# Performance work log

Measured on AMD Instinct MI355X. Metric: run time of the kernel, lower is better.

The kernel has to match this reference:

```python
import jax, jax.numpy as jnp
import numpy as np
import math

N, T, NS, NO, HID = 256, 1000, 10, 10, 64


def gru_seq(x, Wi, Wh, bi, bh):
    # x: [N,T,D] -> hidden states [N,T,HID] (single-layer GRU, h0 = 0)
    xproj = x @ Wi + bi  # [N,T,3H], precompute input projections
    def step(h, xp):
        hp = h @ Wh + bh
        xr, xz, xn = jnp.split(xp, 3, axis=-1)
        hr, hz, hn = jnp.split(hp, 3, axis=-1)
        r = jax.nn.sigmoid(xr + hr)
        z = jax.nn.sigmoid(xz + hz)
        n = jnp.tanh(xn + r * hn)
        h_new = (1.0 - z) * n + z * h
        return h_new, h_new
    h0 = jnp.zeros((x.shape[0], Wh.shape[0]), x.dtype)
    _, hs = jax.lax.scan(step, h0, jnp.swapaxes(xproj, 0, 1))
    return jnp.swapaxes(hs, 0, 1)


def setup_inputs() -> dict:
    key = jax.random.key(0)
    ks = jax.random.split(key, 12)
    D = NO + NS  # GRU input = concat(y, x_hat)
    s = lambda fan: 1.0 / np.sqrt(fan)
    inp = {
        "Yi_batch": jax.random.normal(ks[0], (N, T, NO), jnp.float32),
        "X_hat_batch": jax.random.normal(ks[1], (N, T, NS), jnp.float32),
        # per-sample observation noise covariance: 0.5*I plus small random diagonal
        "Cw_batch": 0.5 * jnp.eye(NO, dtype=jnp.float32)[None] + jnp.eye(NO)[None] * 0.1 * jax.random.uniform(ks[2], (N, 1, 1), jnp.float32),
        "H": jax.random.normal(ks[3], (NO, NS), jnp.float32) * s(NS),
        "mu_w": jnp.zeros((NO, 1), jnp.float32),
        "Wi": jax.random.normal(ks[4], (D, 3 * HID), jnp.float32) * s(D),
        "Wh": jax.random.normal(ks[5], (HID, 3 * HID), jnp.float32) * s(HID),
        "bi": jnp.zeros((3 * HID,), jnp.float32),
        "bh": jnp.zeros((3 * HID,), jnp.float32),
        "W_mu": jax.random.normal(ks[6], (HID, NS), jnp.float32) * s(HID),
        "b_mu": jnp.zeros((NS,), jnp.float32),
        "W_var": jax.random.normal(ks[7], (HID, NS), jnp.float32) * s(HID),
        "b_var": jnp.zeros((NS,), jnp.float32),
    }
    return inp


def reference(Yi_batch, X_hat_batch, Cw_batch, H, mu_w, Wi, Wh, bi, bh, W_mu, b_mu, W_var, b_var):
    n_obs = Yi_batch.shape[-1]
    Tlen = Yi_batch.shape[1]
    # RNN: mu and (positive) vars per time step
    hs = gru_seq(jnp.concatenate([Yi_batch, X_hat_batch], axis=-1), Wi, Wh, bi, bh)
    mu_prev = hs @ W_mu + b_mu                       # [N,T,NS]
    var_prev = jax.nn.softplus(hs @ W_var + b_var)   # [N,T,NS] diag of L_xt_yt_prev
    # marginal over y: mu_y = H mu_prev + mu_w ; L_y = H diag(var) H^T + Cw
    mu_y = jnp.einsum('ij,ntj->nti', H, mu_prev) + mu_w[:, 0]
    HLH = jnp.einsum('ij,ntj,kj->ntik', H, var_prev, H)   # [N,T,NO,NO]
    L_y = HLH + Cw_batch[:, None]                          # broadcast Cw over time
    e = Yi_batch - mu_y
    # Gaussian log-likelihood via Cholesky (L_y is SPD)
    chol = jnp.linalg.cholesky(L_y)
    logdet = 2.0 * jnp.sum(jnp.log(jnp.diagonal(chol, axis1=-2, axis2=-1)), axis=-1)  # [N,T]
    sol = jnp.linalg.solve(L_y, e[..., None])[..., 0]
    quad = jnp.sum(e * sol, axis=-1)                       # [N,T]
    logprob = (-0.5 * n_obs * Tlen * math.log(2.0 * math.pi)
               - 0.5 * jnp.sum(logdet, axis=1)
               - 0.5 * jnp.sum(quad, axis=1))              # [N]
    return jnp.mean(logprob / (Tlen * n_obs))
```

## Files before the change

kernel.cpp:

```cpp
#include <hip/hip_runtime.h>
#include <math.h>

#define BN 256
#define TT 1000
#define NO 10
#define NS 10
#define HID 64
#define DIN 20
#define G3 192
#define GS 8
#define NG 125
#define SPW 16
#define NBLK (BN / SPW)

using bf16x8 = __attribute__((ext_vector_type(8))) short;
using f32x4  = __attribute__((ext_vector_type(4))) float;

__device__ __forceinline__ float rcpf(float x) { return __builtin_amdgcn_rcpf(x); }
__device__ __forceinline__ void sync_lds() {
    asm volatile("s_waitcnt lgkmcnt(0)\n\ts_barrier" ::: "memory");
}
__device__ __forceinline__ unsigned cvt_pk_bf16(float a, float b) {
    unsigned r;
    asm("v_cvt_pk_bf16_f32 %0, %1, %2" : "=v"(r) : "v"(a), "v"(b));
    return r;
}
__device__ __forceinline__ short f2bf(float f) {
    unsigned u = __float_as_uint(f);
    return (short)((u + 0x7fffu + ((u >> 16) & 1u)) >> 16);
}
#define MFMA16 __builtin_amdgcn_mfma_f32_16x16x32_bf16

__device__ __forceinline__ void stage16(ushort* wp, float2 L0, float2 L1,
                                        float2 L2, float2 L3, float2 L4) {
    uint4 a, b;
    a.x = cvt_pk_bf16(L0.x, L0.y);
    a.y = cvt_pk_bf16(L1.x, L1.y);
    a.z = cvt_pk_bf16(L2.x, 0.f);
    a.w = 0u;
    b.x = cvt_pk_bf16(L2.y, L3.x);
    b.y = cvt_pk_bf16(L3.y, L4.x);
    b.z = cvt_pk_bf16(L4.y, 0.f);
    b.w = 0u;
    *(uint4*)(wp)     = a;
    *(uint4*)(wp + 8) = b;
}

__global__ __launch_bounds__(256)
void gru_mfma(const float* __restrict__ Yi, const float* __restrict__ Xh,
              const float* __restrict__ Wi, const float* __restrict__ Wh,
              const float* __restrict__ bi, const float* __restrict__ bh,
              const float* __restrict__ Wmu, const float* __restrict__ Wvar,
              float* __restrict__ mv_out) {
    const int tid = threadIdx.x;
    const int lane = tid & 63;
    const int w   = tid >> 6;
    const int l15 = lane & 15;
    const int lg  = lane >> 4;
    const int n0  = blockIdx.x * SPW;

    __shared__ __align__(16) ushort hb[2][16 * 64];
    __shared__ __align__(16) ushort xb[2][GS][16][32];

    const int u = 16 * w + l15;
    bf16x8 Bxr, Bxz, Bxn, Bhr0, Bhr1, Bhz0, Bhz1, Bhn0, Bhn1;
#pragma unroll
    for (int e = 0; e < 8; ++e) {
        const int d = lg * 5 + e;
        Bxr[e] = (e < 5) ? f2bf(Wi[d * G3 + u])       : (short)0;
        Bxz[e] = (e < 5) ? f2bf(Wi[d * G3 + 64 + u])  : (short)0;
        Bxn[e] = (e < 5) ? f2bf(Wi[d * G3 + 128 + u]) : (short)0;
        const int k0 = lg * 8 + e, k1 = 32 + lg * 8 + e;
        Bhr0[e] = f2bf(Wh[k0 * G3 + u]);       Bhr1[e] = f2bf(Wh[k1 * G3 + u]);
        Bhz0[e] = f2bf(Wh[k0 * G3 + 64 + u]);  Bhz1[e] = f2bf(Wh[k1 * G3 + 64 + u]);
        Bhn0[e] = f2bf(Wh[k0 * G3 + 128 + u]); Bhn1[e] = f2bf(Wh[k1 * G3 + 128 + u]);
    }
    bf16x8 Bmv0 = {}, Bmv1 = {};
    if (w < 2) {
        const int c = 16 * w + l15;
#pragma unroll
        for (int e = 0; e < 8; ++e) {
            const int k0 = lg * 8 + e, k1 = 32 + lg * 8 + e;
            float v0 = 0.f, v1 = 0.f;
            if (c < 10)      { v0 = Wmu[k0 * NS + c];        v1 = Wmu[k1 * NS + c]; }
            else if (c < 20) { v0 = Wvar[k0 * NS + (c - 10)]; v1 = Wvar[k1 * NS + (c - 10)]; }
            Bmv0[e] = f2bf(v0); Bmv1[e] = f2bf(v1);
        }
    }
    const float br  = bi[u] + bh[u];
    const float bz  = bi[64 + u] + bh[64 + u];
    const float bnx = bi[128 + u];
    const float bnh = bh[128 + u];

    const int hro0 = l15 * 64 + (((0 + lg) ^ (l15 & 7)) << 3);
    const int hro1 = l15 * 64 + (((4 + lg) ^ (l15 & 7)) << 3);
    int hwo[4];
#pragma unroll
    for (int r = 0; r < 4; ++r) {
        const int s = 4 * lg + r;
        hwo[r] = s * 64 + ((((u >> 3)) ^ (s & 7)) << 3) + (u & 7);
    }

    const int ss   = tid >> 4;
    const int ii   = tid & 15;
    const int st_t = ii >> 1;
    const int sh   = ii & 1;
    const float* src_base = sh ? (Xh + (size_t)(n0 + ss) * TT * NS)
                               : (Yi + (size_t)(n0 + ss) * TT * NO);

    {
        ushort* hf = (ushort*)hb;
        for (int i = tid; i < 2 * 16 * 64; i += 256) hf[i] = 0;
        const float* p = src_base + (size_t)st_t * 10;
        const float2 L0 = *(const float2*)(p);
        const float2 L1 = *(const float2*)(p + 2);
        const float2 L2 = *(const float2*)(p + 4);
        const float2 L3 = *(const float2*)(p + 6);
        const float2 L4 = *(const float2*)(p + 8);
        stage16(&xb[0][st_t][ss][sh * 16], L0, L1, L2, L3, L4);
        sync_lds();
    }

    float hreg[4] = {0.f, 0.f, 0.f, 0.f};

#pragma unroll 1
    for (int g = 0; g < NG; ++g) {
        const int bq = g & 1;
        float2 L0, L1, L2, L3, L4;
        const bool do_ld = (g + 1 < NG);
        if (do_ld) {
            const float* p = src_base + (size_t)((g + 1) * GS + st_t) * 10;
            L0 = *(const float2*)(p);     L1 = *(const float2*)(p + 2);
            L2 = *(const float2*)(p + 4); L3 = *(const float2*)(p + 6);
            L4 = *(const float2*)(p + 8);
        }

#pragma unroll
        for (int st = 0; st < GS; ++st) {
            const int p = st & 1;
            const int t = 8 * g + st;
            const bf16x8 xa = *(const bf16x8*)&xb[bq][st][l15][lg * 8];
            const bf16x8 h0 = *(const bf16x8*)((const ushort*)hb[p] + hro0);
            const bf16x8 h1 = *(const bf16x8*)((const ushort*)hb[p] + hro1);

            f32x4 ar = {br, br, br, br}, az = {bz, bz, bz, bz};
            f32x4 ax = {bnx, bnx, bnx, bnx}, ah = {bnh, bnh, bnh, bnh};
            ar = MFMA16(xa, Bxr, ar, 0, 0, 0);
            az = MFMA16(xa, Bxz, az, 0, 0, 0);
            ax = MFMA16(xa, Bxn, ax, 0, 0, 0);
            ar = MFMA16(h0, Bhr0, ar, 0, 0, 0);
            az = MFMA16(h0, Bhz0, az, 0, 0, 0);
            ah = MFMA16(h0, Bhn0, ah, 0, 0, 0);
            ar = MFMA16(h1, Bhr1, ar, 0, 0, 0);
            az = MFMA16(h1, Bhz1, az, 0, 0, 0);
            ah = MFMA16(h1, Bhn1, ah, 0, 0, 0);
            if (w < 2) {
                f32x4 amv = {0.f, 0.f, 0.f, 0.f};
                amv = MFMA16(h0, Bmv0, amv, 0, 0, 0);
                amv = MFMA16(h1, Bmv1, amv, 0, 0, 0);
                if (t > 0) {
#pragma unroll
                    for (int r = 0; r < 4; ++r) {
                        const size_t smp = (size_t)(n0 + 4 * lg + r);
                        if (w == 0)
                            mv_out[(smp * TT + (t - 1)) * DIN + l15] = amv[r];
                        else if (l15 < 4)
                            mv_out[(smp * TT + (t - 1)) * DIN + 16 + l15] = amv[r];
                    }
                }
            }
#pragma unroll
            for (int r = 0; r < 4; ++r) {
                const float rr  = rcpf(1.f + __expf(-ar[r]));
                const float zz  = rcpf(1.f + __expf(-az[r]));
                const float pre = fmaf(rr, ah[r], ax[r]);
                const float e2  = __expf(2.f * pre);
                const float nn  = 1.f - 2.f * rcpf(e2 + 1.f);
                hreg[r] = fmaf(zz, hreg[r] - nn, nn);
            }
            const unsigned pk01 = cvt_pk_bf16(hreg[0], hreg[1]);
            const unsigned pk23 = cvt_pk_bf16(hreg[2], hreg[3]);
            ushort* hw = (ushort*)hb[p ^ 1];
            hw[hwo[0]] = (ushort)pk01;
            hw[hwo[1]] = (ushort)(pk01 >> 16);
            hw[hwo[2]] = (ushort)pk23;
            hw[hwo[3]] = (ushort)(pk23 >> 16);
            if (st == GS - 1 && do_ld)
                stage16(&xb[bq ^ 1][st_t][ss][sh * 16], L0, L1, L2, L3, L4);
            sync_lds();
        }
    }

    if (w < 2) {
        const bf16x8 h0 = *(const bf16x8*)((const ushort*)hb[0] + hro0);
        const bf16x8 h1 = *(const bf16x8*)((const ushort*)hb[0] + hro1);
        f32x4 amv = {0.f, 0.f, 0.f, 0.f};
        amv = MFMA16(h0, Bmv0, amv, 0, 0, 0);
        amv = MFMA16(h1, Bmv1, amv, 0, 0, 0);
#pragma unroll
        for (int r = 0; r < 4; ++r) {
            const size_t smp = (size_t)(n0 + 4 * lg + r);
            if (w == 0)
                mv_out[(smp * TT + (TT - 1)) * DIN + l15] = amv[r];
            else if (l15 < 4)
                mv_out[(smp * TT + (TT - 1)) * DIN + 16 + l15] = amv[r];
        }
    }
}

__global__ void init_out(float* out) {
    out[0] = -0.918938533204672742f;
}

__global__ __launch_bounds__(256)
void lik_phase2(const float* __restrict__ Yi, const float* __restrict__ Cw,
                const float* __restrict__ Hm, const float* __restrict__ mu_w,
                const float* __restrict__ b_mu, const float* __restrict__ b_var,
                const float* __restrict__ mv_in, float* __restrict__ out) {
    __shared__ float sH[NO * NS];
    __shared__ float smw[NO], sbm[NS], sbv[NS];
    __shared__ float ssum[4];
    const int tid = threadIdx.x;
    if (tid < NO * NS) sH[tid] = Hm[tid];
    if (tid < NO) smw[tid] = mu_w[tid];
    if (tid < NS) { sbm[tid] = b_mu[tid]; sbv[tid] = b_var[tid]; }
    __syncthreads();

    const int gid = blockIdx.x * 256 + tid;
    float contrib = 0.0f;
    if (gid < BN * TT) {
        const int n = gid / TT;
        const float* mv = mv_in + (size_t)gid * DIN;
        float mu[NS], va[NS];
#pragma unroll
        for (int i = 0; i < NS; ++i) {
            mu[i] = mv[i] + sbm[i];
            float x = mv[NS + i] + sbv[i];
            va[i] = (x > 0.0f) ? (x + log1pf(__expf(-x))) : log1pf(__expf(x));
        }
        const float* y = Yi + (size_t)gid * NO;
        float e[NO];
#pragma unroll
        for (int i = 0; i < NO; ++i) {
            float m = smw[i];
#pragma unroll
            for (int j = 0; j < NS; ++j) m = fmaf(sH[i * NS + j], mu[j], m);
            e[i] = y[i] - m;
        }
        float M[NO][NO];
        const float* cw = Cw + (size_t)n * NO * NO;
#pragma unroll
        for (int i = 0; i < NO; ++i)
#pragma unroll
            for (int j = 0; j <= i; ++j) M[i][j] = cw[i * NO + j];
#pragma unroll
        for (int l = 0; l < NS; ++l) {
            float vl = va[l];
            float hv[NO];
#pragma unroll
            for (int i = 0; i < NO; ++i) hv[i] = sH[i * NS + l];
#pragma unroll
            for (int i = 0; i < NO; ++i) {
                float hvi = hv[i] * vl;
#pragma unroll
                for (int j = 0; j <= i; ++j) M[i][j] = fmaf(hvi, hv[j], M[i][j]);
            }
        }
        float logdet = 0.0f;
        float drs[NO];
#pragma unroll
        for (int j = 0; j < NO; ++j) {
            float d = M[j][j];
#pragma unroll
            for (int k = 0; k < j; ++k) d = fmaf(-M[j][k], M[j][k], d);
            logdet += __logf(d);
            float rs = __frsqrt_rn(d);
            drs[j] = rs;
            M[j][j] = d * rs;
#pragma unroll
            for (int i = j + 1; i < NO; ++i) {
                float v = M[i][j];
#pragma unroll
                for (int k = 0; k < j; ++k) v = fmaf(-M[i][k], M[j][k], v);
                M[i][j] = v * rs;
            }
        }
        float wv[NO];
        float quad = 0.0f;
#pragma unroll
        for (int i = 0; i < NO; ++i) {
            float v = e[i];
#pragma unroll
            for (int k = 0; k < i; ++k) v = fmaf(-M[i][k], wv[k], v);
            wv[i] = v * drs[i] * rcpf(M[i][i] * drs[i]);
            quad = fmaf(wv[i], wv[i], quad);
        }
        const float SCALE = 0.5f / ((float)BN * (float)TT * (float)NO);
        contrib = -(logdet + quad) * SCALE;
    }

#pragma unroll
    for (int off = 32; off > 0; off >>= 1) contrib += __shfl_down(contrib, off);
    if ((tid & 63) == 0) ssum[tid >> 6] = contrib;
    __syncthreads();
    if (tid == 0) {
        float s = ssum[0] + ssum[1] + ssum[2] + ssum[3];
        atomicAdd(out, s);
    }
}

extern "C" void kernel_launch(void* const* d_in, const int* in_sizes, int n_in,
                              void* d_out, int out_size, void* d_ws, size_t ws_size,
                              hipStream_t stream) {
    const float* Yi    = (const float*)d_in[0];
    const float* Xh    = (const float*)d_in[1];
    const float* Cw    = (const float*)d_in[2];
    const float* Hm    = (const float*)d_in[3];
    const float* mu_w  = (const float*)d_in[4];
    const float* Wi    = (const float*)d_in[5];
    const float* Wh    = (const float*)d_in[6];
    const float* bi    = (const float*)d_in[7];
    const float* bh    = (const float*)d_in[8];
    const float* W_mu  = (const float*)d_in[9];
    const float* b_mu  = (const float*)d_in[10];
    const float* W_var = (const float*)d_in[11];
    const float* b_var = (const float*)d_in[12];
    float* out = (float*)d_out;
    float* mv  = (float*)d_ws;

    init_out<<<1, 1, 0, stream>>>(out);
    gru_mfma<<<dim3(NBLK), dim3(256), 0, stream>>>(Yi, Xh, Wi, Wh, bi, bh,
                                                   W_mu, W_var, mv);
    lik_phase2<<<dim3((BN * TT + 255) / 256), dim3(256), 0, stream>>>(
        Yi, Cw, Hm, mu_w, b_mu, b_var, mv, out);
}
```

Measured before the change: 706.7 us.

## Split GRU input projection into a parallel precompute kernel before recurrence

Adds a fully parallel kernel that computes the input projections (x@Wi + bi, with bh folded in for the r/z gates) for all timesteps with MFMA and writes them to workspace in fragment-friendly layout. A new recurrence kernel then only does the h@Wh MFMAs per step, with the precomputed projections loaded two steps ahead as accumulator initialisers. The aim is to shorten the serial critical path of the sequential kernel, at the cost of about 200 MB of extra global traffic and an extra launch. The old fused kernel remains as a fallback when the workspace is too small.

```diff
diff --git a/kernel.cpp b/kernel.cpp
--- a/kernel.cpp
+++ b/kernel.cpp
@@ -30,6 +30,210 @@
     return (short)((u + 0x7fffu + ((u >> 16) & 1u)) >> 16);
 }
 #define MFMA16 __builtin_amdgcn_mfma_f32_16x16x32_bf16
+
+__global__ __launch_bounds__(64)
+void xproj_pre(const float* __restrict__ Yi, const float* __restrict__ Xh,
+               const float* __restrict__ Wi, const float* __restrict__ bi,
+               const float* __restrict__ bh, float* __restrict__ xp) {
+    const int tid = threadIdx.x;
+    const int l15 = tid & 15, lg = tid >> 4;
+    const int g  = blockIdx.x / 125;
+    const int tc = blockIdx.x % 125;
+
+    __shared__ __align__(16) ushort xs[8][16][32];
+
+    bf16x8 B[12];
+    float bc[12];
+#pragma unroll
+    for (int tile = 0; tile < 12; ++tile) {
+        const int u = tile * 16 + l15;
+#pragma unroll
+        for (int e = 0; e < 8; ++e) {
+            const int k = lg * 8 + e;
+            B[tile][e] = (k < 20) ? f2bf(Wi[k * G3 + u]) : (short)0;
+        }
+        bc[tile] = bi[u] + ((u < 128) ? bh[u] : 0.0f);
+    }
+
+    {
+        const int s = tid & 15, tt = tid >> 4;
+#pragma unroll
+        for (int rep = 0; rep < 2; ++rep) {
+            const int t = tt + 4 * rep;
+            const float* yp = Yi + ((size_t)(g * 16 + s) * TT + (tc * 8 + t)) * NO;
+            const float* xq = Xh + ((size_t)(g * 16 + s) * TT + (tc * 8 + t)) * NS;
+            float y[10], x[10];
+#pragma unroll
+            for (int i = 0; i < 10; ++i) { y[i] = yp[i]; x[i] = xq[i]; }
+            uint4 a, b, c;
+            a.x = cvt_pk_bf16(y[0], y[1]); a.y = cvt_pk_bf16(y[2], y[3]);
+            a.z = cvt_pk_bf16(y[4], y[5]); a.w = cvt_pk_bf16(y[6], y[7]);
+            b.x = cvt_pk_bf16(y[8], y[9]); b.y = cvt_pk_bf16(x[0], x[1]);
+            b.z = cvt_pk_bf16(x[2], x[3]); b.w = cvt_pk_bf16(x[4], x[5]);
+            c.x = cvt_pk_bf16(x[6], x[7]); c.y = cvt_pk_bf16(x[8], x[9]);
+            c.z = 0u; c.w = 0u;
+            uint4* wp = (uint4*)&xs[t][s][0];
+            wp[0] = a; wp[1] = b; wp[2] = c; wp[3] = make_uint4(0u, 0u, 0u, 0u);
+        }
+    }
+    sync_lds();
+
+    float* outg = xp + (size_t)g * TT * 3072 + (size_t)(tc * 8) * 3072;
+#pragma unroll
+    for (int t = 0; t < 8; ++t) {
+        const bf16x8 A = *(const bf16x8*)&xs[t][l15][lg * 8];
+        float* outt = outg + (size_t)t * 3072 + lg * 4;
+#pragma unroll
+        for (int tile = 0; tile < 12; ++tile) {
+            f32x4 acc = {bc[tile], bc[tile], bc[tile], bc[tile]};
+            acc = MFMA16(A, B[tile], acc, 0, 0, 0);
+            *(f32x4*)(outt + (size_t)(tile * 16 + l15) * 16) = acc;
+        }
+    }
+}
+
+__global__ __launch_bounds__(256)
+void gru_rec(const float* __restrict__ Wh, const float* __restrict__ bh,
+             const float* __restrict__ Wmu, const float* __restrict__ Wvar,
+             const float* __restrict__ xp, float* __restrict__ mv_out) {
+    const int tid = threadIdx.x;
+    const int lane = tid & 63;
+    const int w   = tid >> 6;
+    const int l15 = lane & 15;
+    const int lg  = lane >> 4;
+    const int g   = blockIdx.x;
+    const int n0  = g * SPW;
+
+    __shared__ __align__(16) ushort hb[2][16 * 64];
+
+    const int u = 16 * w + l15;
+    bf16x8 Bhr0, Bhr1, Bhz0, Bhz1, Bhn0, Bhn1;
+#pragma unroll
+    for (int e = 0; e < 8; ++e) {
+        const int k0 = lg * 8 + e, k1 = 32 + lg * 8 + e;
+        Bhr0[e] = f2bf(Wh[k0 * G3 + u]);       Bhr1[e] = f2bf(Wh[k1 * G3 + u]);
+        Bhz0[e] = f2bf(Wh[k0 * G3 + 64 + u]);  Bhz1[e] = f2bf(Wh[k1 * G3 + 64 + u]);
+        Bhn0[e] = f2bf(Wh[k0 * G3 + 128 + u]); Bhn1[e] = f2bf(Wh[k1 * G3 + 128 + u]);
+    }
+    bf16x8 Bmv0 = {}, Bmv1 = {};
+    if (w < 2) {
+        const int c = 16 * w + l15;
+#pragma unroll
+        for (int e = 0; e < 8; ++e) {
+            const int k0 = lg * 8 + e, k1 = 32 + lg * 8 + e;
+            float v0 = 0.f, v1 = 0.f;
+            if (c < 10)      { v0 = Wmu[k0 * NS + c];        v1 = Wmu[k1 * NS + c]; }
+            else if (c < 20) { v0 = Wvar[k0 * NS + (c - 10)]; v1 = Wvar[k1 * NS + (c - 10)]; }
+            Bmv0[e] = f2bf(v0); Bmv1[e] = f2bf(v1);
+        }
+    }
+    const float bnh = bh[128 + u];
+
+    const int hro0 = l15 * 64 + (((0 + lg) ^ (l15 & 7)) << 3);
+    const int hro1 = l15 * 64 + (((4 + lg) ^ (l15 & 7)) << 3);
+    int hwo[4];
+#pragma unroll
+    for (int r = 0; r < 4; ++r) {
+        const int s = 4 * lg + r;
+        hwo[r] = s * 64 + ((((u >> 3)) ^ (s & 7)) << 3) + (u & 7);
+    }
+
+    {
+        ushort* hf = (ushort*)hb;
+        for (int i = tid; i < 2 * 16 * 64; i += 256) hf[i] = 0;
+    }
+    sync_lds();
+
+    const float* xpg = xp + (size_t)g * TT * 3072;
+    const int xo = u * 16 + 4 * lg;
+    f32x4 xrA = *(const f32x4*)(xpg + xo);
+    f32x4 xzA = *(const f32x4*)(xpg + 1024 + xo);
+    f32x4 xnA = *(const f32x4*)(xpg + 2048 + xo);
+    f32x4 xrB = *(const f32x4*)(xpg + 3072 + xo);
+    f32x4 xzB = *(const f32x4*)(xpg + 3072 + 1024 + xo);
+    f32x4 xnB = *(const f32x4*)(xpg + 3072 + 2048 + xo);
+
+    float hreg[4] = {0.f, 0.f, 0.f, 0.f};
+    const f32x4 z4 = {0.f, 0.f, 0.f, 0.f};
+
+#define STEP(T, XR, XZ, XN)                                                    \
+    {                                                                          \
+        const int t = (T);                                                     \
+        const int p = t & 1;                                                   \
+        const bf16x8 h0 = *(const bf16x8*)((const ushort*)hb[p] + hro0);       \
+        const bf16x8 h1 = *(const bf16x8*)((const ushort*)hb[p] + hro1);       \
+        f32x4 aR = MFMA16(h0, Bhr0, XR, 0, 0, 0);                              \
+        f32x4 bR = MFMA16(h1, Bhr1, z4, 0, 0, 0);                              \
+        f32x4 aZ = MFMA16(h0, Bhz0, XZ, 0, 0, 0);                              \
+        f32x4 bZ = MFMA16(h1, Bhz1, z4, 0, 0, 0);                              \
+        f32x4 aH = MFMA16(h0, Bhn0, (f32x4){bnh, bnh, bnh, bnh}, 0, 0, 0);     \
+        f32x4 bH = MFMA16(h1, Bhn1, z4, 0, 0, 0);                              \
+        const f32x4 axv = XN;                                                  \
+        {                                                                      \
+            const int tl = (t + 2 < TT) ? (t + 2) : (TT - 1);                  \
+            const float* pb = xpg + (size_t)tl * 3072;                         \
+            XR = *(const f32x4*)(pb + xo);                                     \
+            XZ = *(const f32x4*)(pb + 1024 + xo);                              \
+            XN = *(const f32x4*)(pb + 2048 + xo);                              \
+        }                                                                      \
+        if (w < 2) {                                                           \
+            f32x4 amv = MFMA16(h0, Bmv0, z4, 0, 0, 0);                         \
+            amv = MFMA16(h1, Bmv1, amv, 0, 0, 0);                              \
+            if (t > 0) {                                                       \
+                _Pragma("unroll")                                              \
+                for (int r = 0; r < 4; ++r) {                                  \
+                    const size_t smp = (size_t)(n0 + 4 * lg + r);              \
+                    if (w == 0)                                                \
+                        mv_out[(smp * TT + (t - 1)) * DIN + l15] = amv[r];     \
+                    else if (l15 < 4)                                          \
+                        mv_out[(smp * TT + (t - 1)) * DIN + 16 + l15] = amv[r];\
+                }                                                              \
+            }                                                                  \
+        }                                                                      \
+        _Pragma("unroll")                                                      \
+        for (int r = 0; r < 4; ++r) {                                          \
+            const float ar = aR[r] + bR[r];                                    \
+            const float az = aZ[r] + bZ[r];                                    \
+            const float ah = aH[r] + bH[r];                                    \
+            const float rr  = rcpf(1.f + __expf(-ar));                         \
+            const float zz  = rcpf(1.f + __expf(-az));                         \
+            const float pre = fmaf(rr, ah, axv[r]);                            \
+            const float e2  = __expf(2.f * pre);                               \
+            const float nn  = 1.f - 2.f * rcpf(e2 + 1.f);                      \
+            hreg[r] = fmaf(zz, hreg[r] - nn, nn);                              \
+        }                                                                      \
+        const unsigned pk01 = cvt_pk_bf16(hreg[0], hreg[1]);                   \
+        const unsigned pk23 = cvt_pk_bf16(hreg[2], hreg[3]);                   \
+        ushort* hw = (ushort*)hb[p ^ 1];                                       \
+        hw[hwo[0]] = (ushort)pk01;                                             \
+        hw[hwo[1]] = (ushort)(pk01 >> 16);                                     \
+        hw[hwo[2]] = (ushort)pk23;                                             \
+        hw[hwo[3]] = (ushort)(pk23 >> 16);                                     \
+        sync_lds();                                                            \
+    }
+
+#pragma unroll 1
+    for (int tt = 0; tt < TT / 2; ++tt) {
+        STEP(2 * tt,     xrA, xzA, xnA)
+        STEP(2 * tt + 1, xrB, xzB, xnB)
+    }
+#undef STEP
+
+    if (w < 2) {
+        const bf16x8 h0 = *(const bf16x8*)((const ushort*)hb[0] + hro0);
+        const bf16x8 h1 = *(const bf16x8*)((const ushort*)hb[0] + hro1);
+        f32x4 amv = MFMA16(h0, Bmv0, z4, 0, 0, 0);
+        amv = MFMA16(h1, Bmv1, amv, 0, 0, 0);
+#pragma unroll
+        for (int r = 0; r < 4; ++r) {
+            const size_t smp = (size_t)(n0 + 4 * lg + r);
+            if (w == 0)
+                mv_out[(smp * TT + (TT - 1)) * DIN + l15] = amv[r];
+            else if (l15 < 4)
+                mv_out[(smp * TT + (TT - 1)) * DIN + 16 + l15] = amv[r];
+        }
+    }
+}
 
 __device__ __forceinline__ void stage16(ushort* wp, float2 L0, float2 L1,
                                         float2 L2, float2 L3, float2 L4) {
@@ -47,11 +251,11 @@
 }
 
 __global__ __launch_bounds__(256)
-void gru_mfma(const float* __restrict__ Yi, const float* __restrict__ Xh,
-              const float* __restrict__ Wi, const float* __restrict__ Wh,
-              const float* __restrict__ bi, const float* __restrict__ bh,
-              const float* __restrict__ Wmu, const float* __restrict__ Wvar,
-              float* __restrict__ mv_out) {
+void gru_mfma_fb(const float* __restrict__ Yi, const float* __restrict__ Xh,
+                 const float* __restrict__ Wi, const float* __restrict__ Wh,
+                 const float* __restrict__ bi, const float* __restrict__ bh,
+                 const float* __restrict__ Wmu, const float* __restrict__ Wvar,
+                 float* __restrict__ mv_out) {
     const int tid = threadIdx.x;
     const int lane = tid & 63;
     const int w   = tid >> 6;
@@ -328,9 +532,19 @@
     float* out = (float*)d_out;
     float* mv  = (float*)d_ws;
 
+    const size_t mv_f = (size_t)BN * TT * DIN;
+    const size_t xp_f = (size_t)BN * TT * G3;
+    const size_t need = (mv_f + xp_f) * sizeof(float);
+
     init_out<<<1, 1, 0, stream>>>(out);
-    gru_mfma<<<dim3(NBLK), dim3(256), 0, stream>>>(Yi, Xh, Wi, Wh, bi, bh,
-                                                   W_mu, W_var, mv);
+    if (ws_size >= need) {
+        float* xpbuf = mv + mv_f;
+        xproj_pre<<<dim3(NBLK * 125), dim3(64), 0, stream>>>(Yi, Xh, Wi, bi, bh, xpbuf);
+        gru_rec<<<dim3(NBLK), dim3(256), 0, stream>>>(Wh, bh, W_mu, W_var, xpbuf, mv);
+    } else {
+        gru_mfma_fb<<<dim3(NBLK), dim3(256), 0, stream>>>(Yi, Xh, Wi, Wh, bi, bh,
+                                                          W_mu, W_var, mv);
+    }
     lik_phase2<<<dim3((BN * TT + 255) / 256), dim3(256), 0, stream>>>(
         Yi, Cw, Hm, mu_w, b_mu, b_var, mv, out);
 }
```

After: 774.6 us. 9.6% more time.
